# Optimization experiments

Hardware: AMD Instinct MI355X
Metric: run time of the kernel (lower is better)

The kernel has to match this reference:

```python
import jax, jax.numpy as jnp
import numpy as np

N_EMBD = 2048
DIM_ATT = 2048
HEAD_SIZE = 64
N_HEAD = DIM_ATT // HEAD_SIZE
D_MIX = 32
D_DECAY = 64
N_LAYER = 24
LAYER_ID = 12
EPS = 1e-5 * 8.0 ** 2  # GroupNorm eps with head_size_divisor=8


def setup_inputs() -> dict:
    key = jax.random.key(0)
    ks = jax.random.split(key, 10)
    B, T, C = 4, 2048, N_EMBD
    r0 = LAYER_ID / (N_LAYER - 1)          # ratio_0_to_1
    r1 = 1.0 - LAYER_ID / N_LAYER          # ratio_1_to_almost0
    ddd = (np.arange(C, dtype=np.float64) / C)
    f32 = np.float32
    time_maa_x = (1.0 - ddd ** r1).astype(f32)[None, None, :]
    time_maa_w = (1.0 - ddd ** r1).astype(f32)[None, None, :]
    time_maa_k = (1.0 - ddd ** r1).astype(f32)[None, None, :]
    time_maa_v = (1.0 - (ddd ** r1 + 0.3 * r0)).astype(f32)[None, None, :]
    time_maa_r = (1.0 - ddd ** (0.5 * r1)).astype(f32)[None, None, :]
    time_maa_g = (1.0 - ddd ** (0.5 * r1)).astype(f32)[None, None, :]
    n = np.arange(DIM_ATT, dtype=np.float64)
    decay_speed = (-6.0 + 5.0 * (n / (DIM_ATT - 1)) ** (0.7 + 1.3 * r0)).astype(f32)
    time_decay = decay_speed[None, None, :]
    zig = ((n + 1) % 3 - 1) * 0.1
    time_faaaa = (r0 * (1.0 - n / (DIM_ATT - 1)) + zig).astype(f32).reshape(N_HEAD, HEAD_SIZE)
    u = lambda k, sh: jax.random.uniform(k, sh, jnp.float32, -0.01, 0.01)
    inp = {
        'x': jax.random.normal(ks[0], (B, T, C), jnp.float32),
        'time_maa_x': jnp.asarray(time_maa_x), 'time_maa_w': jnp.asarray(time_maa_w),
        'time_maa_k': jnp.asarray(time_maa_k), 'time_maa_v': jnp.asarray(time_maa_v),
        'time_maa_r': jnp.asarray(time_maa_r), 'time_maa_g': jnp.asarray(time_maa_g),
        'time_maa_w1': u(ks[1], (C, D_MIX * 5)),
        'time_maa_w2': u(ks[2], (5, D_MIX, C)),
        'time_decay': jnp.asarray(time_decay),
        'time_decay_w1': u(ks[3], (C, D_DECAY)),
        'time_decay_w2': u(ks[4], (D_DECAY, DIM_ATT)),
        'time_faaaa': jnp.asarray(time_faaaa),
        'W_r': jax.random.normal(ks[5], (DIM_ATT, C), jnp.float32) * 0.02,
        'W_k': jax.random.normal(ks[6], (DIM_ATT, C), jnp.float32) * 0.02,
        'W_v': jax.random.normal(ks[7], (DIM_ATT, C), jnp.float32) * 0.02,
        'W_g': jax.random.normal(ks[8], (DIM_ATT, C), jnp.float32) * 0.02,
        'W_o': jax.random.normal(ks[9], (C, DIM_ATT), jnp.float32) * 0.02,
        'ln_gamma': jnp.ones((DIM_ATT,), jnp.float32),
        'ln_beta': jnp.zeros((DIM_ATT,), jnp.float32),
    }
    return inp


def _wkv6(r, k, v, w, u):
    # r,k,v,w: (B,T,H,N); u: (H,N). decay = exp(-exp(w)) applied per key-dim j.
    B, T, H, N = r.shape
    decay = jnp.exp(-jnp.exp(w))

    def step(S, inp):  # S: (B,H,N,N) indexed [b,h,j,i]
        r_t, k_t, v_t, d_t = inp  # each (B,H,N)
        kv = k_t[..., :, None] * v_t[..., None, :]          # (B,H,N,N)
        y = jnp.einsum('bhj,bhji->bhi', r_t, S + u[None, :, :, None] * kv)
        return d_t[..., None] * S + kv, y

    seq = (r.transpose(1, 0, 2, 3), k.transpose(1, 0, 2, 3),
           v.transpose(1, 0, 2, 3), decay.transpose(1, 0, 2, 3))
    S0 = jnp.zeros((B, H, N, N), r.dtype)
    _, ys = jax.lax.scan(step, S0, seq)                      # (T,B,H,N)
    return ys.transpose(1, 0, 2, 3)                          # (B,T,H,N)


def reference(x, time_maa_x, time_maa_w, time_maa_k, time_maa_v, time_maa_r, time_maa_g,
              time_maa_w1, time_maa_w2, time_decay, time_decay_w1, time_decay_w2,
              time_faaaa, W_r, W_k, W_v, W_g, W_o, ln_gamma, ln_beta):
    B, T, C = x.shape
    H, N = time_faaaa.shape
    xx = jnp.concatenate([jnp.zeros_like(x[:, :1]), x[:, :-1]], axis=1) - x  # time_shift - x
    xxx = x + xx * time_maa_x
    D = time_maa_w2.shape[1]
    a = jnp.tanh(xxx @ time_maa_w1).reshape(B, T, 5, D)
    m = jnp.einsum('btfd,fdc->fbtc', a, time_maa_w2)
    mw, mk, mv, mr, mg = m[0], m[1], m[2], m[3], m[4]
    xw = x + xx * (time_maa_w + mw)
    xk = x + xx * (time_maa_k + mk)
    xv = x + xx * (time_maa_v + mv)
    xr = x + xx * (time_maa_r + mr)
    xg = x + xx * (time_maa_g + mg)
    r = xr @ W_r.T
    k = xk @ W_k.T
    v = xv @ W_v.T
    g = jax.nn.silu(xg @ W_g.T)
    w = time_decay + jnp.tanh(xw @ time_decay_w1) @ time_decay_w2
    y = _wkv6(r.reshape(B, T, H, N), k.reshape(B, T, H, N),
              v.reshape(B, T, H, N), w.reshape(B, T, H, N), time_faaaa)
    # GroupNorm with H groups over channel dim
    mean = y.mean(-1, keepdims=True)
    var = y.var(-1, keepdims=True)
    yn = ((y - mean) * jax.lax.rsqrt(var + EPS)).reshape(B, T, H * N)
    yn = yn * ln_gamma + ln_beta
    return (yn * g) @ W_o.T
```

## Files before the change

kernel.cpp:

```cpp
#include <hip/hip_runtime.h>
#include <hip/hip_bf16.h>
#include <math.h>

#define B_ 4
#define T_ 2048
#define C_ 2048
#define H_ 32
#define BT_ 8192
#define WELE 4194304L
#define BTC  16777216L
#define NCH_ 16
#define TC_  128
#define GNT  32

typedef unsigned short u16;
typedef __bf16 bf16x8 __attribute__((ext_vector_type(8)));
typedef float  f32x4  __attribute__((ext_vector_type(4)));

__device__ __forceinline__ u16 f2b(float f){
  __hip_bfloat16 h = __float2bfloat16(f);
  return *reinterpret_cast<u16*>(&h);
}
__device__ __forceinline__ float b2f(u16 u){
  __hip_bfloat16 h; *reinterpret_cast<u16*>(&h) = u;
  return __bfloat162float(h);
}
__device__ __forceinline__ float bits2f(unsigned u){
  union { unsigned u; float f; } c; c.u = u; return c.f;
}

__device__ __forceinline__ void async_copy16(const u16* gptr, u16* lptr){
  __builtin_amdgcn_global_load_lds(
      (const __attribute__((address_space(1))) unsigned int*)gptr,
      (__attribute__((address_space(3))) unsigned int*)lptr,
      16, 0, 0);
}

__device__ __forceinline__ void unpack4(const u16* __restrict__ gp, float* out){
  const uint2 raw = *(const uint2*)gp;
  out[0] = bits2f(raw.x << 16); out[1] = bits2f(raw.x & 0xffff0000u);
  out[2] = bits2f(raw.y << 16); out[3] = bits2f(raw.y & 0xffff0000u);
}

__global__ __launch_bounds__(256) void cvt1(const float* __restrict__ src,
                                            u16* __restrict__ dst)
{
  const long i = ((long)blockIdx.x*256 + threadIdx.x)*4;
  const float4 v = *(const float4*)(src + i);
  ushort4 o = { f2b(v.x), f2b(v.y), f2b(v.z), f2b(v.w) };
  *(ushort4*)(dst + i) = o;
}

__global__ __launch_bounds__(256) void tposeA(const float* __restrict__ src,
    u16* __restrict__ dst, int R, int Cc, int Npad)
{
  const long idx = (long)blockIdx.x*256 + threadIdx.x;
  if (idx >= (long)Npad * R) return;
  const int n = (int)(idx / R), rr = (int)(idx % R);
  float vv = (n < Cc) ? src[(long)rr * Cc + n] : 0.f;
  dst[idx] = f2b(vv);
}

__global__ __launch_bounds__(256) void tposeW2(const float* __restrict__ src,
                                               u16* __restrict__ dst)
{
  const long idx = (long)blockIdx.x*256 + threadIdx.x;
  const int f = (int)(idx / 65536);
  const int rem = (int)(idx % 65536);
  const int c = rem >> 5, d = rem & 31;
  dst[idx] = f2b(src[((long)f*32 + d)*2048 + c]);
}

__global__ __launch_bounds__(256) void mixA(const float* __restrict__ x,
    const float* __restrict__ maax, u16* __restrict__ xxx, u16* __restrict__ xxb)
{
  const long i = ((long)blockIdx.x*256 + threadIdx.x) * 4;
  const int c   = (int)(i & (C_-1));
  const int tok = (int)(i >> 11);
  const int t   = tok & (T_-1);
  const float4 xc = *(const float4*)(x + i);
  float4 xp = make_float4(0.f,0.f,0.f,0.f);
  if (t > 0) xp = *(const float4*)(x + i - C_);
  const float4 mx = *(const float4*)(maax + c);
  const float xx0 = xp.x - xc.x, xx1 = xp.y - xc.y;
  const float xx2 = xp.z - xc.z, xx3 = xp.w - xc.w;
  ushort4 ox = { f2b(xx0), f2b(xx1), f2b(xx2), f2b(xx3) };
  ushort4 o3 = { f2b(fmaf(xx0, mx.x, xc.x)), f2b(fmaf(xx1, mx.y, xc.y)),
                 f2b(fmaf(xx2, mx.z, xc.z)), f2b(fmaf(xx3, mx.w, xc.w)) };
  *(ushort4*)(xxb + i) = ox;
  *(ushort4*)(xxx + i) = o3;
}

enum { EPI_BF16=0, EPI_TANH=1, EPI_SILU=2, EPI_MIX=3, EPI_DECAY=4, EPI_F32=5 };

template<int EPI>
__global__ __launch_bounds__(256) void gemm_bt(
    const u16* __restrict__ A, int lda,
    const u16* __restrict__ Bm, int ldb, int K,
    void* __restrict__ Out, int ldo,
    const float* __restrict__ aux0, const u16* __restrict__ aux1,
    const float* __restrict__ aux2)
{
  __shared__ u16 As[128*32];
  __shared__ u16 Bs[128*32];
  const int tid = threadIdx.x;
  const int w = tid >> 6, lane = tid & 63;
  const int m0 = blockIdx.y * 128, n0 = blockIdx.x * 128;
  const int wm = w >> 1, wn = w & 1;
  const int rowA = lane >> 2, chunk = lane & 3;
  f32x4 acc[4][4];
  #pragma unroll
  for (int i=0;i<4;i++)
    #pragma unroll
    for (int j=0;j<4;j++) acc[i][j] = (f32x4){0.f,0.f,0.f,0.f};

  for (int k0 = 0; k0 < K; k0 += 32){
    #pragma unroll
    for (int s=0; s<2; s++){
      const int seg = w*2 + s;
      const int row = seg*16 + rowA;
      async_copy16(A  + (long)(m0+row)*lda + k0 + chunk*8, As + seg*512);
      async_copy16(Bm + (long)(n0+row)*ldb + k0 + chunk*8, Bs + seg*512);
    }
    __syncthreads();
    const int kq = (lane >> 4) * 8;
    const int lr16 = lane & 15;
    bf16x8 af[4], bfr[4];
    #pragma unroll
    for (int mt=0; mt<4; mt++)
      af[mt] = *(const bf16x8*)(As + (wm*64 + mt*16 + lr16)*32 + kq);
    #pragma unroll
    for (int nt=0; nt<4; nt++)
      bfr[nt] = *(const bf16x8*)(Bs + (wn*64 + nt*16 + lr16)*32 + kq);
    #pragma unroll
    for (int mt=0; mt<4; mt++)
      #pragma unroll
      for (int nt=0; nt<4; nt++)
        acc[mt][nt] = __builtin_amdgcn_mfma_f32_16x16x32_bf16(af[mt], bfr[nt], acc[mt][nt], 0, 0, 0);
    __syncthreads();
  }

  const int cr = lane & 15, cq = lane >> 4;
  #pragma unroll
  for (int mt=0; mt<4; mt++){
    #pragma unroll
    for (int nt=0; nt<4; nt++){
      #pragma unroll
      for (int rr=0; rr<4; rr++){
        const int row = m0 + wm*64 + mt*16 + cq*4 + rr;
        const int col = n0 + wn*64 + nt*16 + cr;
        const long oi = (long)row*ldo + col;
        const float val = acc[mt][nt][rr];
        if constexpr (EPI == EPI_F32){
          ((float*)Out)[oi] = val;
        } else if constexpr (EPI == EPI_BF16){
          ((u16*)Out)[oi] = f2b(val);
        } else if constexpr (EPI == EPI_TANH){
          ((u16*)Out)[oi] = f2b(tanhf(val));
        } else if constexpr (EPI == EPI_SILU){
          ((u16*)Out)[oi] = f2b(val / (1.f + expf(-val)));
        } else if constexpr (EPI == EPI_MIX){
          const float xv  = aux0[oi];
          const float xxv = b2f(aux1[oi]);
          ((u16*)Out)[oi] = f2b(fmaf(xxv, aux2[col] + val, xv));
        } else {
          ((float*)Out)[oi] = expf(-expf(val + aux0[col]));
        }
      }
    }
  }
}

template<int EPI>
__global__ __launch_bounds__(512) void gemm256(
    const u16* __restrict__ A, const u16* __restrict__ Bm,
    void* __restrict__ Out, int ldo)
{
  __shared__ u16 lds[65536];
  const int tid  = threadIdx.x;
  const int w    = tid >> 6, lane = tid & 63;
  const int wm   = w >> 2, wn = w & 3;
  const long m0  = (long)blockIdx.y * 256;
  const long n0  = (long)blockIdx.x * 256;

  auto stage_half = [&](u16* ldsbase, const u16* gb){
    const int rsub = lane >> 3;
    const int c16  = (lane & 7) ^ rsub;
    #pragma unroll
    for (int r2 = 0; r2 < 2; ++r2){
      const int row = (r2*8 + w)*8 + rsub;
      async_copy16(gb + (long)row*2048 + c16*8,
                   ldsbase + (r2*8 + w)*512);
    }
  };
  auto stage = [&](int t, int half){
    if (t >= GNT) return;
    const int b = t & 1;
    const long k0 = (long)t * 64;
    if      (half == 0) stage_half(lds + 32768 + b*16384,        Bm + n0*2048 + k0);
    else if (half == 1) stage_half(lds + 32768 + b*16384 + 8192, Bm + (n0+128)*2048 + k0);
    else if (half == 2) stage_half(lds + b*16384,                A  + m0*2048 + k0);
    else                stage_half(lds + b*16384 + 8192,         A  + (m0+128)*2048 + k0);
  };

  const int lr16 = lane & 15;
  const int kq   = lane >> 4;
  auto aslot = [&](int buf, int row, int c16)->const u16*{
    return lds + buf*16384 + row*64 + ((c16 ^ (row & 7)) << 3);
  };
  auto bslot = [&](int buf, int row, int c16)->const u16*{
    return lds + 32768 + buf*16384 + row*64 + ((c16 ^ (row & 7)) << 3);
  };

  f32x4 acc[8][4];
  #pragma unroll
  for (int i=0;i<8;i++)
    #pragma unroll
    for (int j=0;j<4;j++) acc[i][j] = (f32x4){0.f,0.f,0.f,0.f};

  stage(0,0); stage(0,1); stage(0,2); stage(0,3);
  stage(1,0); stage(1,1); stage(1,2);
  asm volatile("s_waitcnt vmcnt(6)");
  asm volatile("" ::: "memory");
  __builtin_amdgcn_s_barrier();

  for (int t = 0; t < GNT; ++t){
    const int buf = t & 1;
    bf16x8 bfr[4][2];
    #pragma unroll
    for (int p = 0; p < 4; ++p){
      if (p == 0){
        #pragma unroll
        for (int nt=0; nt<4; nt++)
          #pragma unroll
          for (int kk=0; kk<2; kk++)
            bfr[nt][kk] = *(const bf16x8*)bslot(buf, wn*64 + nt*16 + lr16, kk*4 + kq);
      }
      bf16x8 af[2][2];
      #pragma unroll
      for (int i=0; i<2; i++)
        #pragma unroll
        for (int kk=0; kk<2; kk++)
          af[i][kk] = *(const bf16x8*)aslot(buf, wm*128 + (2*p+i)*16 + lr16, kk*4 + kq);
      if (p == 0) stage(t+1, 3);
      else        stage(t+2, p-1);
      if (p == 3){
        if (t <= GNT-3) asm volatile("s_waitcnt vmcnt(6)");
        else            asm volatile("s_waitcnt vmcnt(0)");
      }
      asm volatile("" ::: "memory");
      __builtin_amdgcn_s_barrier();
      __builtin_amdgcn_s_setprio(1);
      #pragma unroll
      for (int i=0; i<2; i++)
        #pragma unroll
        for (int nt=0; nt<4; nt++)
          #pragma unroll
          for (int kk=0; kk<2; kk++)
            acc[2*p+i][nt] = __builtin_amdgcn_mfma_f32_16x16x32_bf16(
                af[i][kk], bfr[nt][kk], acc[2*p+i][nt], 0, 0, 0);
      __builtin_amdgcn_s_setprio(0);
    }
  }

  const int cr = lane & 15, cq = lane >> 4;
  #pragma unroll
  for (int mt=0; mt<8; mt++){
    #pragma unroll
    for (int nt=0; nt<4; nt++){
      #pragma unroll
      for (int rr=0; rr<4; rr++){
        const long row = m0 + wm*128 + mt*16 + cq*4 + rr;
        const long col = n0 + wn*64 + nt*16 + cr;
        const long oi  = row*ldo + col;
        const float val = acc[mt][nt][rr];
        if constexpr (EPI == EPI_F32){
          ((float*)Out)[oi] = val;
        } else if constexpr (EPI == EPI_BF16){
          ((u16*)Out)[oi] = f2b(val);
        } else {
          ((u16*)Out)[oi] = f2b(val / (1.f + expf(-val)));
        }
      }
    }
  }
}


__global__ __launch_bounds__(256) void wkv_pass1(
    const u16* __restrict__ k, const u16* __restrict__ v,
    const float* __restrict__ dec,
    float* __restrict__ Sbuf, float* __restrict__ Dbuf)
{
  const int blk = blockIdx.x;
  const int c  = blk & (NCH_-1);
  if (c == NCH_-1) return;
  const int bh = blk >> 4;
  const int b = bh >> 5, h = bh & 31;
  const int tid = threadIdx.x;
  const int jg = tid >> 6, lane = tid & 63;
  const int hoff = h * 64;

  float S[16], D[16];
  #pragma unroll
  for (int jj=0;jj<16;jj++){ S[jj]=0.f; D[jj]=1.f; }

  __shared__ float ks[16][64], dsh[16][64], vs[16][64];

  const long base0 = ((long)b * T_) * C_ + hoff;
  const int joff = jg * 16;
  const int stt = tid >> 4;
  const int scc = (tid & 15) * 4;
  const int tA = c * TC_;

  for (int t0 = tA; t0 < tA + TC_; t0 += 16){
    __syncthreads();
    {
      const long gi = base0 + (long)(t0 + stt) * C_ + scc;
      float tmp[4];
      unpack4(k + gi, tmp);  *(float4*)&ks[stt][scc]  = *(float4*)tmp;
      unpack4(v + gi, tmp);  *(float4*)&vs[stt][scc]  = *(float4*)tmp;
      *(float4*)&dsh[stt][scc] = *(const float4*)(dec + gi);
    }
    __syncthreads();
    #pragma unroll 2
    for (int tt = 0; tt < 16; tt++){
      float kv[16], dv[16];
      #pragma unroll
      for (int q=0;q<4;q++){
        *(float4*)(kv+q*4) = *(const float4*)&ks[tt][joff+q*4];
        *(float4*)(dv+q*4) = *(const float4*)&dsh[tt][joff+q*4];
      }
      const float vi = vs[tt][lane];
      #pragma unroll
      for (int jj=0;jj<16;jj++){
        S[jj] = fmaf(dv[jj], S[jj], kv[jj]*vi);
        D[jj] *= dv[jj];
      }
    }
  }
  float* Sp = Sbuf + (long)blk*4096 + (long)joff*64 + lane;
  #pragma unroll
  for (int jj=0;jj<16;jj++) Sp[jj*64] = S[jj];
  if (lane == 0){
    float* Dp = Dbuf + (long)blk*64 + joff;
    #pragma unroll
    for (int jj=0;jj<16;jj++) Dp[jj] = D[jj];
  }
}

__global__ __launch_bounds__(256) void wkv_pass2(
    float* __restrict__ Sbuf, const float* __restrict__ Dbuf)
{
  const int bh = blockIdx.x >> 4;
  const int f  = ((blockIdx.x & 15) << 8) + threadIdx.x;
  const int j = f >> 6;
  float cur = 0.f;
  const long sbase = (long)bh * NCH_ * 4096 + f;
  const long dbase = (long)bh * NCH_ * 64 + j;
  for (int c = 0; c < NCH_-1; c++){
    float* Sp = Sbuf + sbase + (long)c*4096;
    const float tmp = *Sp;
    *Sp = cur;
    cur = fmaf(Dbuf[dbase + (long)c*64], cur, tmp);
  }
  Sbuf[sbase + (long)(NCH_-1)*4096] = cur;
}

__global__ __launch_bounds__(256) void wkv_pass3(
    const u16* __restrict__ r, const u16* __restrict__ k, const u16* __restrict__ v,
    const float* __restrict__ dec, const float* __restrict__ faaaa,
    const float* __restrict__ gam, const float* __restrict__ bet,
    const u16* __restrict__ g, u16* __restrict__ act,
    const float* __restrict__ Sbuf)
{
  const int blk = blockIdx.x;
  const int c  = blk & (NCH_-1);
  const int bh = blk >> 4;
  const int b = bh >> 5, h = bh & 31;
  const int tid = threadIdx.x;
  const int jg = tid >> 6, lane = tid & 63;
  const int hoff = h * 64;
  const int joff = jg * 16;

  float S[16];
  {
    const float* Sp = Sbuf + (long)blk*4096 + (long)joff*64 + lane;
    #pragma unroll
    for (int jj=0;jj<16;jj++) S[jj] = Sp[jj*64];
  }
  float u[16];
  #pragma unroll
  for (int jj=0;jj<16;jj++) u[jj] = faaaa[hoff + jg*16 + jj];
  const float gmv = gam[hoff + lane], btv = bet[hoff + lane];

  __shared__ float rs[16][64], ks[16][64], dsh[16][64], vs[16][64];
  __shared__ float yred[16][4][64];

  const long base0 = ((long)b * T_) * C_ + hoff;
  const int stt = tid >> 4;
  const int scc = (tid & 15) * 4;
  const int tA = c * TC_;

  for (int t0 = tA; t0 < tA + TC_; t0 += 16){
    __syncthreads();
    {
      const long gi = base0 + (long)(t0 + stt) * C_ + scc;
      float tmp[4];
      unpack4(r + gi, tmp);  *(float4*)&rs[stt][scc]  = *(float4*)tmp;
      unpack4(k + gi, tmp);  *(float4*)&ks[stt][scc]  = *(float4*)tmp;
      unpack4(v + gi, tmp);  *(float4*)&vs[stt][scc]  = *(float4*)tmp;
      *(float4*)&dsh[stt][scc] = *(const float4*)(dec + gi);
    }
    __syncthreads();
    #pragma unroll 2
    for (int tt = 0; tt < 16; tt++){
      float rv[16], kv[16], dv[16];
      #pragma unroll
      for (int q=0;q<4;q++){
        *(float4*)(rv+q*4) = *(const float4*)&rs[tt][joff+q*4];
        *(float4*)(kv+q*4) = *(const float4*)&ks[tt][joff+q*4];
        *(float4*)(dv+q*4) = *(const float4*)&dsh[tt][joff+q*4];
      }
      const float vi = vs[tt][lane];
      float yp = 0.f;
      #pragma unroll
      for (int jj=0;jj<16;jj++){
        const float p = kv[jj] * vi;
        yp = fmaf(rv[jj], fmaf(u[jj], p, S[jj]), yp);
        S[jj] = fmaf(dv[jj], S[jj], p);
      }
      yred[tt][jg][lane] = yp;
    }
    __syncthreads();
    #pragma unroll
    for (int q=0;q<4;q++){
      const int tt = jg*4 + q;
      const float y = yred[tt][0][lane] + yred[tt][1][lane]
                    + yred[tt][2][lane] + yred[tt][3][lane];
      float s1 = y, s2 = y*y;
      #pragma unroll
      for (int off=32; off>0; off>>=1){
        s1 += __shfl_xor(s1, off, 64);
        s2 += __shfl_xor(s2, off, 64);
      }
      const float mean = s1 * (1.f/64.f);
      const float var  = s2 * (1.f/64.f) - mean*mean;
      const float yn   = (y - mean) * rsqrtf(var + 6.4e-4f);
      const long  oi   = base0 + (long)(t0 + tt) * C_ + lane;
      const float o    = (yn * gmv + btv) * b2f(g[oi]);
      act[oi] = f2b(o);
    }
  }
}

extern "C" void kernel_launch(void* const* d_in, const int* in_sizes, int n_in,
                              void* d_out, int out_size, void* d_ws, size_t ws_size,
                              hipStream_t stream)
{
  const float* x     = (const float*)d_in[0];
  const float* tmx   = (const float*)d_in[1];
  const float* maaf[5] = {(const float*)d_in[2], (const float*)d_in[3],
                          (const float*)d_in[4], (const float*)d_in[5],
                          (const float*)d_in[6]};
  const float* w1    = (const float*)d_in[7];
  const float* w2    = (const float*)d_in[8];
  const float* td    = (const float*)d_in[9];
  const float* tdw1  = (const float*)d_in[10];
  const float* tdw2  = (const float*)d_in[11];
  const float* faaaa = (const float*)d_in[12];
  const float* Wmat[5] = {(const float*)d_in[13], (const float*)d_in[14],
                          (const float*)d_in[15], (const float*)d_in[16],
                          (const float*)d_in[17]};
  const float* ln_g  = (const float*)d_in[18];
  const float* ln_b  = (const float*)d_in[19];

  char* p = (char*)d_ws;
  auto take = [&](size_t bytes)->char*{
    char* q = p; p += (bytes + 255) & ~(size_t)255; return q;
  };
  u16*   w1t  = (u16*)take(256L*2048*2);
  u16*   w2t  = (u16*)take(5L*2048*32*2);
  u16*   wd1t = (u16*)take(128L*2048*2);
  u16*   wd2t = (u16*)take(2048L*64*2);
  u16*   wcur = (u16*)take(WELE*2);
  u16*   xxx  = (u16*)take(BTC*2);
  u16*   xxb  = (u16*)take(BTC*2);
  u16*   abuf = (u16*)take((long)BT_*256*2);
  u16*   hbuf = (u16*)take((long)BT_*128*2);
  u16*   kbuf = (u16*)take(BTC*2);
  u16*   vbuf = (u16*)take(BTC*2);
  u16*   gbuf = (u16*)take(BTC*2);
  u16*   mixbuf = xxx;
  u16*   rbuf   = xxb;
  u16*   act    = kbuf;
  float* dcy    = (float*)d_out;
  float* Sbuf   = (float*)mixbuf;
  float* Dbuf   = (float*)hbuf;
  (void)in_sizes; (void)n_in; (void)out_size; (void)ws_size;

  tposeA <<<2048, 256, 0, stream>>>(w1,   w1t,  2048, 160, 256);
  tposeW2<<<1280, 256, 0, stream>>>(w2,   w2t);
  tposeA <<<1024, 256, 0, stream>>>(tdw1, wd1t, 2048, 64, 128);
  tposeA <<<512,  256, 0, stream>>>(tdw2, wd2t, 64, 2048, 2048);

  mixA<<<16384, 256, 0, stream>>>(x, tmx, xxx, xxb);

  gemm_bt<EPI_TANH><<<dim3(2,64), 256, 0, stream>>>(xxx, 2048, w1t, 2048, 2048,
      abuf, 256, nullptr, nullptr, nullptr);

  gemm_bt<EPI_MIX><<<dim3(16,64), 256, 0, stream>>>(abuf + 0*32, 256,
      w2t + 0L*65536, 32, 32, mixbuf, 2048, x, xxb, maaf[0]);
  gemm_bt<EPI_TANH><<<dim3(1,64), 256, 0, stream>>>(mixbuf, 2048, wd1t, 2048, 2048,
      hbuf, 128, nullptr, nullptr, nullptr);
  gemm_bt<EPI_DECAY><<<dim3(16,64), 256, 0, stream>>>(hbuf, 128, wd2t, 64, 64,
      dcy, 2048, td, nullptr, nullptr);

  gemm_bt<EPI_MIX><<<dim3(16,64), 256, 0, stream>>>(abuf + 1*32, 256,
      w2t + 1L*65536, 32, 32, mixbuf, 2048, x, xxb, maaf[1]);
  cvt1<<<4096, 256, 0, stream>>>(Wmat[1], wcur);
  gemm256<EPI_BF16><<<dim3(8,32), 512, 0, stream>>>(mixbuf, wcur, kbuf, 2048);

  gemm_bt<EPI_MIX><<<dim3(16,64), 256, 0, stream>>>(abuf + 2*32, 256,
      w2t + 2L*65536, 32, 32, mixbuf, 2048, x, xxb, maaf[2]);
  cvt1<<<4096, 256, 0, stream>>>(Wmat[2], wcur);
  gemm256<EPI_BF16><<<dim3(8,32), 512, 0, stream>>>(mixbuf, wcur, vbuf, 2048);

  gemm_bt<EPI_MIX><<<dim3(16,64), 256, 0, stream>>>(abuf + 4*32, 256,
      w2t + 4L*65536, 32, 32, mixbuf, 2048, x, xxb, maaf[4]);
  cvt1<<<4096, 256, 0, stream>>>(Wmat[3], wcur);
  gemm256<EPI_SILU><<<dim3(8,32), 512, 0, stream>>>(mixbuf, wcur, gbuf, 2048);

  gemm_bt<EPI_MIX><<<dim3(16,64), 256, 0, stream>>>(abuf + 3*32, 256,
      w2t + 3L*65536, 32, 32, mixbuf, 2048, x, xxb, maaf[3]);
  cvt1<<<4096, 256, 0, stream>>>(Wmat[0], wcur);
  gemm256<EPI_BF16><<<dim3(8,32), 512, 0, stream>>>(mixbuf, wcur, rbuf, 2048);

  wkv_pass1<<<128*NCH_, 256, 0, stream>>>(kbuf, vbuf, dcy, Sbuf, Dbuf);
  wkv_pass2<<<128*NCH_, 256, 0, stream>>>(Sbuf, Dbuf);
  wkv_pass3<<<128*NCH_, 256, 0, stream>>>(rbuf, kbuf, vbuf, dcy, faaaa,
      ln_g, ln_b, gbuf, act, Sbuf);

  cvt1<<<4096, 256, 0, stream>>>(Wmat[4], wcur);
  gemm256<EPI_F32><<<dim3(8,32), 512, 0, stream>>>(act, wcur, d_out, 2048);
}
```

Measured before the change: 1.033 ms.

## Rewrite WKV chunk-state pass as decay-scaled k outer-product sum

The first WKV pass no longer runs the sequential recurrence S = d*S + k*v per timestep. It now computes suffix products of the decay within the chunk, pre-scales k by them, and accumulates a plain sum of outer products k̃·v over the 128 timesteps. The whole chunk is staged in shared memory in a single stage, with v copied asynchronously, which removes the per-16-step barrier loop and the per-step decay multiply. In exchange it uses more shared memory, holds 32 decay values per thread in registers, and multiplies long runs of decays together, which could change rounding or underflow behaviour.

```diff
diff --git a/kernel.cpp b/kernel.cpp
--- a/kernel.cpp
+++ b/kernel.cpp
@@ -298,55 +298,68 @@
   const int bh = blk >> 4;
   const int b = bh >> 5, h = bh & 31;
   const int tid = threadIdx.x;
-  const int jg = tid >> 6, lane = tid & 63;
+  const int g = tid >> 6, lane = tid & 63;
   const int hoff = h * 64;
-
-  float S[16], D[16];
-  #pragma unroll
-  for (int jj=0;jj<16;jj++){ S[jj]=0.f; D[jj]=1.f; }
-
-  __shared__ float ks[16][64], dsh[16][64], vs[16][64];
-
   const long base0 = ((long)b * T_) * C_ + hoff;
-  const int joff = jg * 16;
-  const int stt = tid >> 4;
-  const int scc = (tid & 15) * 4;
   const int tA = c * TC_;
 
-  for (int t0 = tA; t0 < tA + TC_; t0 += 16){
-    __syncthreads();
-    {
-      const long gi = base0 + (long)(t0 + stt) * C_ + scc;
-      float tmp[4];
-      unpack4(k + gi, tmp);  *(float4*)&ks[stt][scc]  = *(float4*)tmp;
-      unpack4(v + gi, tmp);  *(float4*)&vs[stt][scc]  = *(float4*)tmp;
-      *(float4*)&dsh[stt][scc] = *(const float4*)(dec + gi);
-    }
-    __syncthreads();
-    #pragma unroll 2
-    for (int tt = 0; tt < 16; tt++){
-      float kv[16], dv[16];
-      #pragma unroll
-      for (int q=0;q<4;q++){
-        *(float4*)(kv+q*4) = *(const float4*)&ks[tt][joff+q*4];
-        *(float4*)(dv+q*4) = *(const float4*)&dsh[tt][joff+q*4];
-      }
-      const float vi = vs[tt][lane];
-      #pragma unroll
-      for (int jj=0;jj<16;jj++){
-        S[jj] = fmaf(dv[jj], S[jj], kv[jj]*vi);
-        D[jj] *= dv[jj];
-      }
-    }
+  __shared__ float kts[128][64];
+  __shared__ u16   vsh[128][64];
+  __shared__ float Gp[4][64];
+
+  #pragma unroll
+  for (int rd = 0; rd < 4; ++rd){
+    const int row0 = (rd*4 + g) * 8;
+    async_copy16(v + base0 + (long)(tA + row0 + (lane>>3))*C_ + (lane&7)*8,
+                 &vsh[row0][0]);
+  }
+
+  float d[32];
+  float gp = 1.f;
+  #pragma unroll
+  for (int tau = 0; tau < 32; ++tau){
+    d[tau] = dec[base0 + (long)(tA + g*32 + tau)*C_ + lane];
+    gp *= d[tau];
+  }
+  Gp[g][lane] = gp;
+  __syncthreads();
+  float CS = 1.f;
+  #pragma unroll
+  for (int gg = 0; gg < 4; ++gg)
+    if (gg > g) CS *= Gp[gg][lane];
+  if (g == 0){
+    Dbuf[(long)blk*64 + lane] =
+        Gp[0][lane]*Gp[1][lane]*Gp[2][lane]*Gp[3][lane];
+  }
+  {
+    float R = CS;
+    #pragma unroll
+    for (int tau = 31; tau >= 0; --tau){
+      const float kv = b2f(k[base0 + (long)(tA + g*32 + tau)*C_ + lane]);
+      kts[g*32 + tau][lane] = kv * R;
+      R *= d[tau];
+    }
+  }
+  __syncthreads();
+
+  const int joff = g * 16;
+  float S[16];
+  #pragma unroll
+  for (int jj=0;jj<16;jj++) S[jj]=0.f;
+  #pragma unroll 4
+  for (int t = 0; t < TC_; ++t){
+    float kv[16];
+    #pragma unroll
+    for (int q=0;q<4;q++)
+      *(float4*)(kv+q*4) = *(const float4*)&kts[t][joff+q*4];
+    const float vi = b2f(vsh[t][lane]);
+    #pragma unroll
+    for (int jj=0;jj<16;jj++)
+      S[jj] = fmaf(kv[jj], vi, S[jj]);
   }
   float* Sp = Sbuf + (long)blk*4096 + (long)joff*64 + lane;
   #pragma unroll
   for (int jj=0;jj<16;jj++) Sp[jj*64] = S[jj];
-  if (lane == 0){
-    float* Dp = Dbuf + (long)blk*64 + joff;
-    #pragma unroll
-    for (int jj=0;jj<16;jj++) Dp[jj] = D[jj];
-  }
 }
 
 __global__ __launch_bounds__(256) void wkv_pass2(
```

Measured after the change: 1.030 ms. About the same (-0.3%).
